# Kernel optimization log

Measured on AMD Instinct MI355X. Metric: run time of the kernel, lower is better.

The kernel has to match this reference:

```python
import jax, jax.numpy as jnp
import numpy as np

UPPER = 0.4
LOWER = 0.1
BG_RATIO = 1.0
NCLS = 20
BACKGROUND = NCLS
SIGMA = 10.0          # SmoothL1Loss(10)
MAX_POS = 2048        # fixed capacity for positive RoIs (jit-friendly)
NEGATIVE = -2
NEITHER = -1


def bbox_overlaps(b1, b2):
    """Pairwise IoU, py-faster-rcnn +1 pixel convention. b1 [L,4], b2 [M,4] -> [L,M]."""
    a1 = (b1[:, 2] - b1[:, 0] + 1.0) * (b1[:, 3] - b1[:, 1] + 1.0)  # [L]
    a2 = (b2[:, 2] - b2[:, 0] + 1.0) * (b2[:, 3] - b2[:, 1] + 1.0)  # [M]
    iw = jnp.clip(jnp.minimum(b1[:, None, 2], b2[None, :, 2]) -
                  jnp.maximum(b1[:, None, 0], b2[None, :, 0]) + 1.0, 0.0)
    ih = jnp.clip(jnp.minimum(b1[:, None, 3], b2[None, :, 3]) -
                  jnp.maximum(b1[:, None, 1], b2[None, :, 1]) + 1.0, 0.0)
    inter = iw * ih
    return inter / (a1[:, None] + a2[None, :] - inter)


def smooth_l1(d):
    s2 = SIGMA * SIGMA
    ad = jnp.abs(d)
    return jnp.where(ad < 1.0 / s2, 0.5 * s2 * d * d, ad - 0.5 / s2)


def match(pred, gt):
    """Faithful port of match(): same assignment order (upper -> gt-argmax -> lower)."""
    L = pred.shape[0]
    M = gt.shape[0]
    ov = bbox_overlaps(pred, gt)                       # [L, M]
    best_p = ov.max(axis=1)
    idx_p = ov.argmax(axis=1).astype(jnp.int32)
    ret = jnp.full((L,), NEITHER, dtype=jnp.int32)
    ret = jnp.where(best_p >= UPPER, idx_p, ret)
    idx_g = ov.argmax(axis=0)                          # [M] best roi per gt
    ret = ret.at[idx_g].set(jnp.arange(M, dtype=jnp.int32))
    ret = jnp.where(best_p < LOWER, NEGATIVE, ret)     # applied last, as in torch
    return ret


def reference(rois, cls_scores, bbox_deltas, gt_boxes, gt_cls):
    L, C = cls_scores.shape
    boxes = rois[:, 1:]                                # drop batch index column
    score_idx = jnp.argmax(cls_scores, axis=1)         # [L] predicted class per roi
    deltas = bbox_deltas.reshape(L, C, 4)
    deltas = jnp.take_along_axis(deltas, score_idx[:, None, None], axis=1)[:, 0, :]
    pred = boxes + deltas                              # [L, 4]
    gt = gt_boxes[0]                                   # [M, 4]

    matches = match(pred, gt)                          # [L] int32
    pos = matches >= 0
    neg = matches == NEGATIVE
    num_pos = pos.sum()

    # --- negative sampling: randperm(neg)[:bg_num], done via random ranks ---
    bg_num = jnp.round(num_pos.astype(jnp.float32) * BG_RATIO).astype(jnp.int32)
    u = jax.random.uniform(jax.random.key(42), (L,))
    rank = jnp.zeros((L,), jnp.int32).at[jnp.argsort(jnp.where(neg, u, 2.0))].set(
        jnp.arange(L, dtype=jnp.int32))
    sel_neg = neg & (rank < bg_num)

    # --- classification loss (mean CE over pos + sampled neg) ---
    labels = jnp.where(pos, gt_cls[jnp.clip(matches, 0)], BACKGROUND)
    w = (pos | sel_neg).astype(cls_scores.dtype)
    logp = jax.nn.log_softmax(cls_scores, axis=1)
    ce = -jnp.take_along_axis(logp, labels[:, None], axis=1)[:, 0]
    cls_loss = (ce * w).sum() / w.sum()

    # --- bbox loss over positives (fixed-capacity gather) ---
    order = jnp.argsort(jnp.where(pos, jnp.arange(L), L + jnp.arange(L)))
    pos_idx = order[:MAX_POS]
    valid = pos[pos_idx].astype(pred.dtype)            # [K]
    pred_pos = pred[pos_idx]                           # [K, 4]
    gt_pos = gt[jnp.clip(matches[pos_idx], 0)]         # [K, 4]
    # original broadcasts pred [P,4] against gt.reshape(P,1,4) -> [P,P,4]
    diff = pred_pos[None, :, :] - gt_pos[:, None, :]   # [K, K, 4]
    pair_w = valid[:, None] * valid[None, :]
    bbox_loss = (smooth_l1(diff) * pair_w[:, :, None]).sum() / 1.0  # norm = ones(1)
    return cls_loss, bbox_loss


def setup_inputs() -> dict:
    key = jax.random.key(0)
    ks = jax.random.split(key, 6)
    L, C, M = 65536, 21, 512
    SCALE = 20000.0
    wh = jax.random.uniform(ks[0], (L, 2), minval=100.0, maxval=300.0)
    xy = jax.random.uniform(ks[1], (L, 2), minval=0.0, maxval=SCALE - 300.0)
    boxes = jnp.concatenate([xy, xy + wh], axis=1)                 # [L,4]
    rois = jnp.concatenate([jnp.zeros((L, 1)), boxes], axis=1)     # [L,5]
    jitter = jax.random.uniform(ks[2], (M, 4), minval=-10.0, maxval=10.0)
    gt_boxes = (boxes[:M] + jitter)[None]                          # [1,M,4], IoU>=0.4 w/ first M rois
    gt_cls = jax.random.randint(ks[3], (M,), 0, NCLS, dtype=jnp.int32)
    cls_scores = jax.random.normal(ks[4], (L, C))
    bbox_deltas = jax.random.normal(ks[5], (L, 4 * C)) * 2.0
    return dict(rois=rois, cls_scores=cls_scores, bbox_deltas=bbox_deltas,
                gt_boxes=gt_boxes, gt_cls=gt_cls)
```

## Files before the change

### kernel.cpp

```cpp
#include <hip/hip_runtime.h>
#include <stdint.h>

typedef unsigned int u32;
typedef unsigned long long u64;

#define F_UPPER 0.4f
#define F_LOWER 0.1f
#define MAX_POS 2048
#define L_SZ 65536
#define M_SZ 512
#define C_SZ 21
#define NBINS 8192
#define BIN_CAP 32
#define OVF_CAP 1024
#define COL_TAG 0xC000000000000000ull

#define CELL_SHIFT 11
#define GRID_W 10

struct State {
  int num_pos;
  int num_neg;
  u32 done;
  u32 _pad;
  double bbox_sum;
};

__device__ __forceinline__ float area_fn(const float4 a) {
#pragma clang fp contract(off)
  return (a.z - a.x + 1.0f) * (a.w - a.y + 1.0f);
}

__device__ __forceinline__ float inter_fn(const float4 a, const float4 b) {
#pragma clang fp contract(off)
  float iw = fminf(a.z, b.z) - fmaxf(a.x, b.x) + 1.0f;
  iw = fmaxf(iw, 0.0f);
  float ih = fminf(a.w, b.w) - fmaxf(a.y, b.y) + 1.0f;
  ih = fmaxf(ih, 0.0f);
  return iw * ih;
}

__device__ __forceinline__ float iou_from_inter(float inter, float a1, float a2) {
#pragma clang fp contract(off)
  return inter * __builtin_amdgcn_rcpf(a1 + a2 - inter);
}

__device__ __forceinline__ float sl1(float d) {
#pragma clang fp contract(off)
  float ad = fabsf(d);
  return (ad < 0.01f) ? (50.0f * d * d) : (ad - 0.005f);
}

__device__ __forceinline__ int cellc(float f) {
  int c = ((int)f) >> CELL_SHIFT;
  return (c < 0) ? 0 : ((c > GRID_W - 1) ? GRID_W - 1 : c);
}

__device__ __forceinline__ u32 rotl(u32 x, int d) { return (x << d) | (x >> (32 - d)); }

__device__ u32 threefry_bits(u32 i, u32 H) {
  u32 x0, x1; bool hi;
  if (i < H) { x0 = i;     x1 = i + H; hi = false; }
  else       { x0 = i - H; x1 = i;     hi = true;  }
  const u32 ks0 = 0u, ks1 = 42u;
  const u32 ks2 = ks0 ^ ks1 ^ 0x1BD11BDAu;
  x0 += ks0; x1 += ks1;
#define RND(r) { x0 += x1; x1 = rotl(x1, r); x1 ^= x0; }
  RND(13) RND(15) RND(26) RND(6)   x0 += ks1; x1 += ks2 + 1u;
  RND(17) RND(29) RND(16) RND(24)  x0 += ks2; x1 += ks0 + 2u;
  RND(13) RND(15) RND(26) RND(6)   x0 += ks0; x1 += ks1 + 3u;
  RND(17) RND(29) RND(16) RND(24)  x0 += ks1; x1 += ks2 + 4u;
  RND(13) RND(15) RND(26) RND(6)   x0 += ks2; x1 += ks0 + 5u;
#undef RND
  return hi ? x1 : x0;
}

__global__ void __launch_bounds__(256) kA(const float* __restrict__ rois,
    const float* __restrict__ scores, const float* __restrict__ deltas,
    const float4* __restrict__ gtb,
    float4* __restrict__ pred, float* __restrict__ lse,
    u64* __restrict__ rowkey, u64* __restrict__ gkey, u32* __restrict__ hist0) {
  __shared__ __align__(16) float ssc[256 * C_SZ];
  __shared__ __align__(16) float sro[256 * 5];
  __shared__ float4 sgt[M_SZ];
  __shared__ u32    sgi[M_SZ];
  __shared__ u32    scnt[128];
  __shared__ u32    soff[130];
  __shared__ u64    scol[M_SZ];
  __shared__ u32    scarry;
  const int tid = threadIdx.x;
  const int b = blockIdx.x;
  const int i = (b << 8) + tid;
  const int lane = tid & 63;
  if (tid < 32) hist0[(b << 5) + tid] = 0u;
  {
    const float4* s4 = (const float4*)(scores + (size_t)(b << 8) * C_SZ);
    float4* d4 = (float4*)ssc;
    for (int k = tid; k < (256 * C_SZ) / 4; k += 256) d4[k] = s4[k];
    const float4* r4 = (const float4*)(rois + (size_t)(b << 8) * 5);
    float4* q4 = (float4*)sro;
    for (int k = tid; k < (256 * 5) / 4; k += 256) q4[k] = r4[k];
  }
  float4 g0 = gtb[tid];
  float4 g1 = gtb[tid + 256];
  if (tid < 128) scnt[tid] = 0u;
  scol[tid] = 0ull; scol[tid + 256] = 0ull;
  __syncthreads();
  const int c0 = cellc(g0.y) * GRID_W + cellc(g0.x);
  const int c1 = cellc(g1.y) * GRID_W + cellc(g1.x);
  atomicAdd(&scnt[c0], 1u);
  atomicAdd(&scnt[c1], 1u);
  __syncthreads();
  if (tid < 128) {
    u32 x = scnt[tid];
    for (int off = 1; off < 64; off <<= 1) {
      u32 t = __shfl_up(x, off, 64);
      if (lane >= off) x += t;
    }
    if (tid == 63) scarry = x;
    soff[tid + 1] = x;
    if (tid == 0) soff[0] = 0u;
  }
  __syncthreads();
  if (tid >= 64 && tid < 128) soff[tid + 1] += scarry;
  __syncthreads();
  if (tid < 128) scnt[tid] = soff[tid];
  __syncthreads();
  {
    u32 p0 = atomicAdd(&scnt[c0], 1u);
    sgt[p0] = g0; sgi[p0] = (u32)tid;
    u32 p1 = atomicAdd(&scnt[c1], 1u);
    sgt[p1] = g1; sgi[p1] = (u32)(tid + 256);
  }
  __syncthreads();
  const float* sr = ssc + tid * C_SZ;
  float mx = sr[0]; int mi = 0;
  for (int j = 1; j < C_SZ; ++j) { float v = sr[j]; if (v > mx) { mx = v; mi = j; } }
  float ssum = 0.0f;
  for (int j = 0; j < C_SZ; ++j) ssum += expf(sr[j] - mx);
  lse[i] = mx + logf(ssum);
  float4 d = *(const float4*)(deltas + (size_t)i * (4 * C_SZ) + 4 * mi);
  const float* r = sro + tid * 5;
  float4 p;
  p.x = r[1] + d.x; p.y = r[2] + d.y; p.z = r[3] + d.z; p.w = r[4] + d.w;
  pred[i] = p;
  const float pa = area_fn(p);
  float rbest = 0.0f; int rbj = 0;
  const int cx0 = cellc(p.x - 322.0f), cx1 = cellc(p.z + 1.0f);
  const int cy0 = cellc(p.y - 322.0f), cy1 = cellc(p.w + 1.0f);
  for (int cy = cy0; cy <= cy1; ++cy) {
    for (int cx = cx0; cx <= cx1; ++cx) {
      const int c = cy * GRID_W + cx;
      const int k1 = (int)soff[c + 1];
      for (int k = (int)soff[c]; k < k1; ++k) {
        float4 g = sgt[k];
        float inter = inter_fn(p, g);
        if (inter > 0.0f) {
          float v = iou_from_inter(inter, pa, area_fn(g));
          int j = (int)sgi[k];
          if (v > rbest) { rbest = v; rbj = j; }
          u64 ck = ((u64)__float_as_uint(v) << 32) | (u32)(0xFFFFFFFFu - (u32)i);
          atomicMax(&scol[j], ck);
        }
      }
    }
  }
  rowkey[i] = (rbest > 0.0f)
      ? (((u64)__float_as_uint(rbest) << 32) | (u32)(0xFFFFFFFFu - (u32)rbj))
      : 0ull;
  __syncthreads();
  for (int j = tid; j < M_SZ; j += 256) {
    u64 c = scol[j];
    if ((c >> 32) != 0ull) atomicMax(&gkey[j], c | COL_TAG);
  }
}

__global__ void __launch_bounds__(256) kB1(const u64* __restrict__ rowkey,
    const u64* __restrict__ gkey, const int* __restrict__ gtc,
    const float* __restrict__ scores, const float* __restrict__ lse,
    const float4* __restrict__ pred, const float4* __restrict__ gtb,
    u32* __restrict__ neg_u, u32* __restrict__ hist0, u64* __restrict__ bins,
    u32* __restrict__ blockcnt, double* __restrict__ posce,
    float4* __restrict__ ppg, float4* __restrict__ gpg, State* st) {
  __shared__ int sscat[256];
  __shared__ int swsum[4], sncnt[4];
  __shared__ double sdacc[4];
  const int tid = threadIdx.x, b = blockIdx.x;
  const int lane = tid & 63, wid = tid >> 6;
  if (b == 0 && tid == 0) { st->done = 0u; st->bbox_sum = 0.0; }
  sscat[tid] = -1;
  __syncthreads();
  for (int g = tid; g < M_SZ; g += 256) {
    u64 key = gkey[g];
    int pidx = (int)(0xFFFFFFFFu - (u32)key);
    if ((pidx >> 8) == b) atomicMax(&sscat[pidx & 255], g);
  }
  __syncthreads();
  const int i = (b << 8) + tid;
  u64 rk = rowkey[i];
  float best = __uint_as_float((u32)(rk >> 32));
  int idxp = (int)(0xFFFFFFFFu - (u32)rk);
  int m;
  if (best < F_LOWER) m = -2;
  else {
    int s = sscat[tid];
    m = (s >= 0) ? s : ((best >= F_UPPER) ? idxp : -1);
  }
  u32 ub = threefry_bits((u32)i, L_SZ >> 1) >> 9;
  neg_u[i] = (m == -2) ? ub : 0xFFFFFFFFu;
  float ce = 0.0f;
  if (m >= 0) {
    ce = lse[i] - scores[(size_t)i * C_SZ + gtc[m]];
  } else if (m == -2) {
    u32 bin = ub >> 10;
    u32 pos = atomicAdd(&hist0[bin], 1u);
    if (pos < BIN_CAP) bins[(size_t)bin * BIN_CAP + pos] = ((u64)ub << 16) | (u32)i;
  }
  const int flag = (m >= 0) ? 1 : 0;
  int incl = flag;
#pragma unroll
  for (int off = 1; off < 64; off <<= 1) {
    int x = __shfl_up(incl, off, 64);
    if (lane >= off) incl += x;
  }
  u64 baln = __ballot(m == -2);
  double acc = (double)ce;
  for (int off = 32; off > 0; off >>= 1) acc += __shfl_down(acc, off, 64);
  if (lane == 63) swsum[wid] = incl;
  if (lane == 0) { sncnt[wid] = __popcll(baln); sdacc[wid] = acc; }
  __syncthreads();
  int wbase = 0;
  for (int w = 0; w < wid; ++w) wbase += swsum[w];
  if (flag) {
    int lrank = wbase + incl - flag;
    ppg[(b << 8) + lrank] = pred[i];
    gpg[(b << 8) + lrank] = gtb[m];
  }
  if (tid == 0) {
    u32 cp = (u32)(swsum[0] + swsum[1] + swsum[2] + swsum[3]);
    u32 cn = (u32)(sncnt[0] + sncnt[1] + sncnt[2] + sncnt[3]);
    blockcnt[b] = cp | (cn << 16);
    posce[b] = sdacc[0] + sdacc[1] + sdacc[2] + sdacc[3];
  }
}

__device__ __forceinline__ int rank_src(const int* sscan, int r) {
  int lo = 0, hi = 255;
  while (lo < hi) { int mid = (lo + hi) >> 1; if (sscan[mid] > r) hi = mid; else lo = mid + 1; }
  return lo;
}

__global__ void __launch_bounds__(256) kBC2(const float4* __restrict__ ppg,
    const float4* __restrict__ gpg, const u32* __restrict__ blockcnt,
    const u32* __restrict__ hist0, const u64* __restrict__ bins,
    const u32* __restrict__ neg_u, const float* __restrict__ scores,
    const float* __restrict__ lse, const double* __restrict__ posce,
    double* __restrict__ negce, State* st, float* __restrict__ out) {
  __shared__ int sscan[256];
  __shared__ int scp[256];
  __shared__ int sncnt[4];
  __shared__ double sdacc[4];
  __shared__ int s_d, s_kk, s_cnt;
  __shared__ u32 s_ovf;
  __shared__ u64 sth;
  __shared__ u64 scand[OVF_CAP];
  __shared__ float4 sj[128];
  __shared__ int s_last;
  const int tid = threadIdx.x, b = blockIdx.x;
  const int lane = tid & 63, wid = tid >> 6;
  u32 v = blockcnt[tid];
  int cp = (int)(v & 0xFFFFu), cn = (int)(v >> 16);
  scp[tid] = cp;
  sscan[tid] = cp;
  {
    int c = cn;
    for (int off = 32; off > 0; off >>= 1) c += __shfl_down(c, off, 64);
    if (lane == 0) sncnt[wid] = c;
  }
  __syncthreads();
  for (int off = 1; off < 256; off <<= 1) {
    int x = (tid >= off) ? sscan[tid - off] : 0;
    __syncthreads();
    sscan[tid] += x;
    __syncthreads();
  }
  const int np = sscan[255];
  const int nn = sncnt[0] + sncnt[1] + sncnt[2] + sncnt[3];
  int n = np; if (n > MAX_POS) n = MAX_POS;
  float4 grow; bool irow = false;
  const int jb = (b & 15) << 7;
  if (b < 128) {
    if (tid < 128) {
      int rr = jb + tid;
      if (rr < n) {
        int s = rank_src(sscan, rr);
        int local = rr - (sscan[s] - scp[s]);
        sj[tid] = ppg[(s << 8) + local];
      } else {
        sj[tid] = make_float4(0.f, 0.f, 0.f, 0.f);
      }
    }
    const int ii = ((b >> 4) << 8) + tid;
    if (ii < n) {
      int s = rank_src(sscan, ii);
      int local = ii - (sscan[s] - scp[s]);
      grow = gpg[(s << 8) + local];
      irow = true;
    }
  }
  __syncthreads();
  u64 thresh = ~0ull;
  if (np < nn) {
    const uint4* h4 = (const uint4*)hist0;
    u32 loc[32]; int tsum = 0;
#pragma unroll
    for (int r = 0; r < 8; ++r) {
      uint4 hv = h4[tid * 8 + r];
      loc[r*4] = hv.x; loc[r*4+1] = hv.y; loc[r*4+2] = hv.z; loc[r*4+3] = hv.w;
      tsum += (int)(hv.x + hv.y + hv.z + hv.w);
    }
    sscan[tid] = tsum;
    __syncthreads();
    for (int off = 1; off < 256; off <<= 1) {
      int x = (tid >= off) ? sscan[tid - off] : 0;
      __syncthreads();
      sscan[tid] += x;
      __syncthreads();
    }
    int incl2 = sscan[tid], excl2 = incl2 - tsum;
    if (np >= excl2 && np < incl2) {
      int kk = np - excl2; int d = 0, c = 0;
#pragma unroll
      for (int r = 0; r < 32; ++r) {
        if (kk < (int)loc[r]) { d = tid * 32 + r; c = (int)loc[r]; break; }
        kk -= (int)loc[r];
      }
      s_d = d; s_kk = kk; s_cnt = c;
    }
    if (tid == 0) s_ovf = 0;
    __syncthreads();
    const int d = s_d, kk = s_kk, cnt = s_cnt;
    if (cnt <= BIN_CAP) {
      if (tid < cnt) scand[tid] = bins[(size_t)d * BIN_CAP + tid];
      __syncthreads();
      if (tid < cnt) {
        u64 key = scand[tid];
        int rank = 0;
        for (int u = 0; u < cnt; ++u) rank += (scand[u] < key) ? 1 : 0;
        if (rank == kk) sth = key;
      }
    } else {
      for (int t = tid; t < L_SZ; t += 256) {
        u32 u = neg_u[t];
        if (u != 0xFFFFFFFFu && (int)(u >> 10) == d) {
          u32 pos = atomicAdd(&s_ovf, 1u);
          if (pos < OVF_CAP) scand[pos] = ((u64)u << 16) | (u32)t;
        }
      }
      __syncthreads();
      int c2 = (int)s_ovf; if (c2 > OVF_CAP) c2 = OVF_CAP;
      for (int t = tid; t < c2; t += 256) {
        u64 key = scand[t];
        int rank = 0;
        for (int u = 0; u < c2; ++u) rank += (scand[u] < key) ? 1 : 0;
        if (rank == kk) sth = key;
      }
    }
    __syncthreads();
    thresh = sth;
  }
  {
    const int i = (b << 8) + tid;
    u32 u = neg_u[i];
    double acc = 0.0;
    if (u != 0xFFFFFFFFu) {
      u64 key = ((u64)u << 16) | (u32)i;
      if (key < thresh)
        acc = (double)(lse[i] - scores[(size_t)i * C_SZ + (C_SZ - 1)]);
    }
    for (int off = 32; off > 0; off >>= 1) acc += __shfl_down(acc, off, 64);
    if (lane == 0) sdacc[wid] = acc;
    __syncthreads();
    if (tid == 0) negce[b] = sdacc[0] + sdacc[1] + sdacc[2] + sdacc[3];
  }
  __syncthreads();
  if (b < 128) {
    double pacc = 0.0;
    if (irow) {
      int jend = n - jb; if (jend > 128) jend = 128;
      for (int j = 0; j < jend; ++j) {
        float4 p4 = sj[j];
        pacc += (double)sl1(p4.x - grow.x);
        pacc += (double)sl1(p4.y - grow.y);
        pacc += (double)sl1(p4.z - grow.z);
        pacc += (double)sl1(p4.w - grow.w);
      }
    }
    for (int off = 32; off > 0; off >>= 1) pacc += __shfl_down(pacc, off, 64);
    if (lane == 0) sdacc[wid] = pacc;
    __syncthreads();
    if (tid == 0)
      atomicAdd(&st->bbox_sum, sdacc[0] + sdacc[1] + sdacc[2] + sdacc[3]);
  }
  if (tid == 0) {
    __threadfence();
    u32 dn = atomicAdd(&st->done, 1u);
    s_last = (dn == 255u) ? 1 : 0;
  }
  __syncthreads();
  if (!s_last) return;
  __threadfence();
  double a = posce[tid] + negce[tid];
  for (int off = 32; off > 0; off >>= 1) a += __shfl_down(a, off, 64);
  if (lane == 0) sdacc[wid] = a;
  __syncthreads();
  if (tid == 0) {
    double ce = sdacc[0] + sdacc[1] + sdacc[2] + sdacc[3];
    double bbs = __hip_atomic_load(&st->bbox_sum, __ATOMIC_ACQUIRE, __HIP_MEMORY_SCOPE_AGENT);
    int nsel = (np < nn) ? np : nn;
    double wsum = (double)(np + nsel);
    out[0] = (float)(ce / wsum);
    out[1] = (float)bbs;
  }
}


extern "C" void kernel_launch(void* const* d_in, const int* in_sizes, int n_in,
                              void* d_out, int out_size, void* d_ws, size_t ws_size,
                              hipStream_t stream) {
  const float* rois   = (const float*)d_in[0];
  const float* scores = (const float*)d_in[1];
  const float* deltas = (const float*)d_in[2];
  const float4* gtb   = (const float4*)d_in[3];
  const int*   gtc    = (const int*)d_in[4];
  float* out = (float*)d_out;

  char* w = (char*)d_ws;
  State* st    = (State*)w;   w += 256;
  u64* gkey    = (u64*)w;     w += (size_t)M_SZ * 8;
  u32* hist0   = (u32*)w;     w += (size_t)NBINS * 4;
  u64* bins    = (u64*)w;     w += (size_t)NBINS * BIN_CAP * 8;
  float4* pred = (float4*)w;  w += (size_t)L_SZ * 16;
  float* lse   = (float*)w;   w += (size_t)L_SZ * 4;
  u64* rowkey  = (u64*)w;     w += (size_t)L_SZ * 8;
  u32* neg_u   = (u32*)w;     w += (size_t)L_SZ * 4;
  float4* ppg  = (float4*)w;  w += (size_t)256 * 256 * 16;
  float4* gpg  = (float4*)w;  w += (size_t)256 * 256 * 16;
  u32* blockcnt= (u32*)w;     w += 256 * 4;
  double* posce= (double*)w;  w += 256 * 8;
  double* negce= (double*)w;  w += 256 * 8;

  kA<<<L_SZ / 256, 256, 0, stream>>>(rois, scores, deltas, gtb, pred, lse, rowkey, gkey, hist0);
  kB1<<<L_SZ / 256, 256, 0, stream>>>(rowkey, gkey, gtc, scores, lse, pred, gtb,
                                      neg_u, hist0, bins, blockcnt, posce, ppg, gpg, st);
  kBC2<<<L_SZ / 256, 256, 0, stream>>>(ppg, gpg, blockcnt, hist0, bins, neg_u,
                                       scores, lse, posce, negce, st, out);
}
```

Measured before the change: 121.1 us.

## Fuse match classification into kA and collapse kB1/kBC2 via candidate list

```diff
diff --git a/kernel.cpp b/kernel.cpp
--- a/kernel.cpp
+++ b/kernel.cpp
@@ -13,16 +13,15 @@
 #define NBINS 8192
 #define BIN_CAP 32
 #define OVF_CAP 1024
+#define CAND_CAP 3072
 #define COL_TAG 0xC000000000000000ull
 
 #define CELL_SHIFT 11
 #define GRID_W 10
 
 struct State {
-  int num_pos;
-  int num_neg;
   u32 done;
-  u32 _pad;
+  u32 cand_cnt;
   double bbox_sum;
 };
 
@@ -79,7 +78,9 @@
     const float* __restrict__ scores, const float* __restrict__ deltas,
     const float4* __restrict__ gtb,
     float4* __restrict__ pred, float* __restrict__ lse,
-    u64* __restrict__ rowkey, u64* __restrict__ gkey, u32* __restrict__ hist0) {
+    u64* __restrict__ rowkey, u64* __restrict__ gkey, u32* __restrict__ hist0,
+    u64* __restrict__ bins, u32* __restrict__ neg_u, u64* __restrict__ cand,
+    State* st) {
   __shared__ __align__(16) float ssc[256 * C_SZ];
   __shared__ __align__(16) float sro[256 * 5];
   __shared__ float4 sgt[M_SZ];
@@ -92,7 +93,6 @@
   const int b = blockIdx.x;
   const int i = (b << 8) + tid;
   const int lane = tid & 63;
-  if (tid < 32) hist0[(b << 5) + tid] = 0u;
   {
     const float4* s4 = (const float4*)(scores + (size_t)(b << 8) * C_SZ);
     float4* d4 = (float4*)ssc;
@@ -168,6 +168,18 @@
   rowkey[i] = (rbest > 0.0f)
       ? (((u64)__float_as_uint(rbest) << 32) | (u32)(0xFFFFFFFFu - (u32)rbj))
       : 0ull;
+  if (rbest < F_LOWER) {
+    u32 ub = threefry_bits((u32)i, L_SZ >> 1) >> 9;
+    neg_u[i] = ub;
+    u32 bin = ub >> 10;
+    u32 pos = atomicAdd(&hist0[bin], 1u);
+    if (pos < BIN_CAP) bins[(size_t)bin * BIN_CAP + pos] = ((u64)ub << 16) | (u32)i;
+  } else {
+    neg_u[i] = 0xFFFFFFFFu;
+    u32 slot = atomicAdd(&st->cand_cnt, 1u);
+    if (slot < CAND_CAP)
+      cand[slot] = ((u64)__float_as_uint(rbest) << 32) | ((u64)(u32)i << 16) | (u32)rbj;
+  }
   __syncthreads();
   for (int j = tid; j < M_SZ; j += 256) {
     u64 c = scol[j];
@@ -175,91 +187,29 @@
   }
 }
 
-__global__ void __launch_bounds__(256) kB1(const u64* __restrict__ rowkey,
+__device__ __forceinline__ int hash_lookup(const u64* shash, u32 pidx) {
+  u32 h = (pidx * 2654435761u) >> 22;
+  for (;;) {
+    u64 cur = shash[h];
+    if (cur == 0ull) return -1;
+    if ((cur >> 16) == (u64)(pidx + 1u)) return (int)(cur & 0xFFFFull);
+    h = (h + 1u) & 1023u;
+  }
+}
+
+__global__ void __launch_bounds__(256) kB(const u64* __restrict__ cand,
     const u64* __restrict__ gkey, const int* __restrict__ gtc,
     const float* __restrict__ scores, const float* __restrict__ lse,
     const float4* __restrict__ pred, const float4* __restrict__ gtb,
-    u32* __restrict__ neg_u, u32* __restrict__ hist0, u64* __restrict__ bins,
-    u32* __restrict__ blockcnt, double* __restrict__ posce,
-    float4* __restrict__ ppg, float4* __restrict__ gpg, State* st) {
-  __shared__ int sscat[256];
-  __shared__ int swsum[4], sncnt[4];
-  __shared__ double sdacc[4];
-  const int tid = threadIdx.x, b = blockIdx.x;
-  const int lane = tid & 63, wid = tid >> 6;
-  if (b == 0 && tid == 0) { st->done = 0u; st->bbox_sum = 0.0; }
-  sscat[tid] = -1;
-  __syncthreads();
-  for (int g = tid; g < M_SZ; g += 256) {
-    u64 key = gkey[g];
-    int pidx = (int)(0xFFFFFFFFu - (u32)key);
-    if ((pidx >> 8) == b) atomicMax(&sscat[pidx & 255], g);
-  }
-  __syncthreads();
-  const int i = (b << 8) + tid;
-  u64 rk = rowkey[i];
-  float best = __uint_as_float((u32)(rk >> 32));
-  int idxp = (int)(0xFFFFFFFFu - (u32)rk);
-  int m;
-  if (best < F_LOWER) m = -2;
-  else {
-    int s = sscat[tid];
-    m = (s >= 0) ? s : ((best >= F_UPPER) ? idxp : -1);
-  }
-  u32 ub = threefry_bits((u32)i, L_SZ >> 1) >> 9;
-  neg_u[i] = (m == -2) ? ub : 0xFFFFFFFFu;
-  float ce = 0.0f;
-  if (m >= 0) {
-    ce = lse[i] - scores[(size_t)i * C_SZ + gtc[m]];
-  } else if (m == -2) {
-    u32 bin = ub >> 10;
-    u32 pos = atomicAdd(&hist0[bin], 1u);
-    if (pos < BIN_CAP) bins[(size_t)bin * BIN_CAP + pos] = ((u64)ub << 16) | (u32)i;
-  }
-  const int flag = (m >= 0) ? 1 : 0;
-  int incl = flag;
-#pragma unroll
-  for (int off = 1; off < 64; off <<= 1) {
-    int x = __shfl_up(incl, off, 64);
-    if (lane >= off) incl += x;
-  }
-  u64 baln = __ballot(m == -2);
-  double acc = (double)ce;
-  for (int off = 32; off > 0; off >>= 1) acc += __shfl_down(acc, off, 64);
-  if (lane == 63) swsum[wid] = incl;
-  if (lane == 0) { sncnt[wid] = __popcll(baln); sdacc[wid] = acc; }
-  __syncthreads();
-  int wbase = 0;
-  for (int w = 0; w < wid; ++w) wbase += swsum[w];
-  if (flag) {
-    int lrank = wbase + incl - flag;
-    ppg[(b << 8) + lrank] = pred[i];
-    gpg[(b << 8) + lrank] = gtb[m];
-  }
-  if (tid == 0) {
-    u32 cp = (u32)(swsum[0] + swsum[1] + swsum[2] + swsum[3]);
-    u32 cn = (u32)(sncnt[0] + sncnt[1] + sncnt[2] + sncnt[3]);
-    blockcnt[b] = cp | (cn << 16);
-    posce[b] = sdacc[0] + sdacc[1] + sdacc[2] + sdacc[3];
-  }
-}
-
-__device__ __forceinline__ int rank_src(const int* sscan, int r) {
-  int lo = 0, hi = 255;
-  while (lo < hi) { int mid = (lo + hi) >> 1; if (sscan[mid] > r) hi = mid; else lo = mid + 1; }
-  return lo;
-}
-
-__global__ void __launch_bounds__(256) kBC2(const float4* __restrict__ ppg,
-    const float4* __restrict__ gpg, const u32* __restrict__ blockcnt,
-    const u32* __restrict__ hist0, const u64* __restrict__ bins,
-    const u32* __restrict__ neg_u, const float* __restrict__ scores,
-    const float* __restrict__ lse, const double* __restrict__ posce,
+    const u32* __restrict__ neg_u, const u32* __restrict__ hist0,
+    const u64* __restrict__ bins, const u64* __restrict__ rowkey,
     double* __restrict__ negce, State* st, float* __restrict__ out) {
+  __shared__ u64 shash[1024];
+  __shared__ u32 cand_if[CAND_CAP];
+  __shared__ u32 posim[MAX_POS];
   __shared__ int sscan[256];
-  __shared__ int scp[256];
-  __shared__ int sncnt[4];
-  __shared__ double sdacc[4];
+  __shared__ int sint[4];
+  __shared__ double sdbl[4];
   __shared__ int s_d, s_kk, s_cnt;
   __shared__ u32 s_ovf;
   __shared__ u64 sth;
@@ -268,47 +218,128 @@
   __shared__ int s_last;
   const int tid = threadIdx.x, b = blockIdx.x;
   const int lane = tid & 63, wid = tid >> 6;
-  u32 v = blockcnt[tid];
-  int cp = (int)(v & 0xFFFFu), cn = (int)(v >> 16);
-  scp[tid] = cp;
-  sscan[tid] = cp;
-  {
-    int c = cn;
-    for (int off = 32; off > 0; off >>= 1) c += __shfl_down(c, off, 64);
-    if (lane == 0) sncnt[wid] = c;
-  }
-  __syncthreads();
-  for (int off = 1; off < 256; off <<= 1) {
-    int x = (tid >= off) ? sscan[tid - off] : 0;
-    __syncthreads();
-    sscan[tid] += x;
-    __syncthreads();
-  }
-  const int np = sscan[255];
-  const int nn = sncnt[0] + sncnt[1] + sncnt[2] + sncnt[3];
-  int n = np; if (n > MAX_POS) n = MAX_POS;
+
+  for (int k = tid; k < 1024; k += 256) shash[k] = 0ull;
+  __syncthreads();
+  for (int g = tid; g < M_SZ; g += 256) {
+    u64 key = gkey[g];
+    if ((key >> 62) != 3ull) continue;
+    u32 pidx = 0xFFFFFFFFu - (u32)key;
+    u64 comb = ((u64)(pidx + 1u) << 16) | (u32)g;
+    u32 h = (pidx * 2654435761u) >> 22;
+    for (;;) {
+      u64 cur = shash[h];
+      if (cur == 0ull) {
+        u64 prev = atomicCAS(&shash[h], 0ull, comb);
+        if (prev == 0ull) break;
+        cur = prev;
+      }
+      if ((cur >> 16) == (u64)(pidx + 1u)) { atomicMax(&shash[h], comb); break; }
+      h = (h + 1u) & 1023u;
+    }
+  }
+  __syncthreads();
+
+  const int C = (int)st->cand_cnt;
+  int np, nn;
+  double posce_loc;
+  if (C <= CAND_CAP) {
+    int cp_loc = 0; double pce = 0.0;
+    for (int c = tid; c < C; c += 256) {
+      u64 e = cand[c];
+      float kb = __uint_as_float((u32)(e >> 32));
+      u32 ci = (u32)(e >> 16) & 0xFFFFu;
+      u32 ixp = (u32)e & 0xFFFFu;
+      int g = hash_lookup(shash, ci);
+      int m = (g >= 0) ? g : ((kb >= F_UPPER) ? (int)ixp : -1);
+      cand_if[c] = (ci << 16) | (m >= 0 ? (((u32)m << 1) | 1u) : 0u);
+      if (m >= 0) {
+        cp_loc++;
+        pce += (double)(lse[ci] - scores[(size_t)ci * C_SZ + gtc[m]]);
+      }
+    }
+    __syncthreads();
+    for (int c = tid; c < C; c += 256) {
+      u32 e = cand_if[c];
+      if (e & 1u) {
+        u32 ci = e >> 16;
+        int r = 0;
+        for (int c2 = 0; c2 < C; ++c2) {
+          u32 e2 = cand_if[c2];
+          r += (int)((e2 & 1u) & (u32)((e2 >> 16) < ci));
+        }
+        if (r < MAX_POS) posim[r] = (ci << 16) | ((e >> 1) & 0x3FFu);
+      }
+    }
+    for (int off = 32; off > 0; off >>= 1) {
+      cp_loc += __shfl_down(cp_loc, off, 64);
+      pce += __shfl_down(pce, off, 64);
+    }
+    if (lane == 0) { sint[wid] = cp_loc; sdbl[wid] = pce; }
+    __syncthreads();
+    np = sint[0] + sint[1] + sint[2] + sint[3];
+    posce_loc = sdbl[0] + sdbl[1] + sdbl[2] + sdbl[3];
+    nn = L_SZ - C;
+  } else {
+    int cp_loc = 0, nn_loc = 0; double pce = 0.0;
+    const int base = tid << 8;
+    for (int k = 0; k < 256; ++k) {
+      int i = base + k;
+      u64 rk = rowkey[i];
+      float best = __uint_as_float((u32)(rk >> 32));
+      if (best < F_LOWER) { nn_loc++; continue; }
+      int ixp = (int)(0xFFFFFFFFu - (u32)rk);
+      int g = hash_lookup(shash, (u32)i);
+      int m = (g >= 0) ? g : ((best >= F_UPPER) ? ixp : -1);
+      if (m >= 0) {
+        cp_loc++;
+        pce += (double)(lse[i] - scores[(size_t)i * C_SZ + gtc[m]]);
+      }
+    }
+    sscan[tid] = cp_loc;
+    __syncthreads();
+    for (int off = 1; off < 256; off <<= 1) {
+      int x = (tid >= off) ? sscan[tid - off] : 0;
+      __syncthreads();
+      sscan[tid] += x;
+      __syncthreads();
+    }
+    np = sscan[255];
+    int r = sscan[tid] - cp_loc;
+    for (int k = 0; k < 256; ++k) {
+      int i = base + k;
+      u64 rk = rowkey[i];
+      float best = __uint_as_float((u32)(rk >> 32));
+      if (best < F_LOWER) continue;
+      int ixp = (int)(0xFFFFFFFFu - (u32)rk);
+      int g = hash_lookup(shash, (u32)i);
+      int m = (g >= 0) ? g : ((best >= F_UPPER) ? ixp : -1);
+      if (m >= 0) { if (r < MAX_POS) posim[r] = ((u32)i << 16) | (u32)m; r++; }
+    }
+    for (int off = 32; off > 0; off >>= 1) {
+      nn_loc += __shfl_down(nn_loc, off, 64);
+      pce += __shfl_down(pce, off, 64);
+    }
+    if (lane == 0) { sint[wid] = nn_loc; sdbl[wid] = pce; }
+    __syncthreads();
+    nn = sint[0] + sint[1] + sint[2] + sint[3];
+    posce_loc = sdbl[0] + sdbl[1] + sdbl[2] + sdbl[3];
+  }
+  __syncthreads();
+
+  int n = (np > MAX_POS) ? MAX_POS : np;
   float4 grow; bool irow = false;
   const int jb = (b & 15) << 7;
   if (b < 128) {
     if (tid < 128) {
       int rr = jb + tid;
-      if (rr < n) {
-        int s = rank_src(sscan, rr);
-        int local = rr - (sscan[s] - scp[s]);
-        sj[tid] = ppg[(s << 8) + local];
-      } else {
-        sj[tid] = make_float4(0.f, 0.f, 0.f, 0.f);
-      }
+      sj[tid] = (rr < n) ? pred[posim[rr] >> 16] : make_float4(0.f, 0.f, 0.f, 0.f);
     }
     const int ii = ((b >> 4) << 8) + tid;
-    if (ii < n) {
-      int s = rank_src(sscan, ii);
-      int local = ii - (sscan[s] - scp[s]);
-      grow = gpg[(s << 8) + local];
-      irow = true;
-    }
-  }
-  __syncthreads();
+    if (ii < n) { grow = gtb[posim[ii] & 0xFFFFu]; irow = true; }
+  }
+  __syncthreads();
+
   u64 thresh = ~0ull;
   if (np < nn) {
     const uint4* h4 = (const uint4*)hist0;
@@ -369,6 +400,7 @@
     __syncthreads();
     thresh = sth;
   }
+
   {
     const int i = (b << 8) + tid;
     u32 u = neg_u[i];
@@ -379,9 +411,9 @@
         acc = (double)(lse[i] - scores[(size_t)i * C_SZ + (C_SZ - 1)]);
     }
     for (int off = 32; off > 0; off >>= 1) acc += __shfl_down(acc, off, 64);
-    if (lane == 0) sdacc[wid] = acc;
-    __syncthreads();
-    if (tid == 0) negce[b] = sdacc[0] + sdacc[1] + sdacc[2] + sdacc[3];
+    if (lane == 0) sdbl[wid] = acc;
+    __syncthreads();
+    if (tid == 0) negce[b] = sdbl[0] + sdbl[1] + sdbl[2] + sdbl[3];
   }
   __syncthreads();
   if (b < 128) {
@@ -397,10 +429,10 @@
       }
     }
     for (int off = 32; off > 0; off >>= 1) pacc += __shfl_down(pacc, off, 64);
-    if (lane == 0) sdacc[wid] = pacc;
+    if (lane == 0) sdbl[wid] = pacc;
     __syncthreads();
     if (tid == 0)
-      atomicAdd(&st->bbox_sum, sdacc[0] + sdacc[1] + sdacc[2] + sdacc[3]);
+      atomicAdd(&st->bbox_sum, sdbl[0] + sdbl[1] + sdbl[2] + sdbl[3]);
   }
   if (tid == 0) {
     __threadfence();
@@ -410,16 +442,16 @@
   __syncthreads();
   if (!s_last) return;
   __threadfence();
-  double a = posce[tid] + negce[tid];
+  double a = negce[tid];
   for (int off = 32; off > 0; off >>= 1) a += __shfl_down(a, off, 64);
-  if (lane == 0) sdacc[wid] = a;
+  if (lane == 0) sdbl[wid] = a;
   __syncthreads();
   if (tid == 0) {
-    double ce = sdacc[0] + sdacc[1] + sdacc[2] + sdacc[3];
+    double negsum = sdbl[0] + sdbl[1] + sdbl[2] + sdbl[3];
     double bbs = __hip_atomic_load(&st->bbox_sum, __ATOMIC_ACQUIRE, __HIP_MEMORY_SCOPE_AGENT);
     int nsel = (np < nn) ? np : nn;
     double wsum = (double)(np + nsel);
-    out[0] = (float)(ce / wsum);
+    out[0] = (float)((posce_loc + negsum) / wsum);
     out[1] = (float)bbs;
   }
 }
@@ -437,22 +469,19 @@
 
   char* w = (char*)d_ws;
   State* st    = (State*)w;   w += 256;
+  u32* hist0   = (u32*)w;     w += (size_t)NBINS * 4;
   u64* gkey    = (u64*)w;     w += (size_t)M_SZ * 8;
-  u32* hist0   = (u32*)w;     w += (size_t)NBINS * 4;
   u64* bins    = (u64*)w;     w += (size_t)NBINS * BIN_CAP * 8;
   float4* pred = (float4*)w;  w += (size_t)L_SZ * 16;
   float* lse   = (float*)w;   w += (size_t)L_SZ * 4;
   u64* rowkey  = (u64*)w;     w += (size_t)L_SZ * 8;
   u32* neg_u   = (u32*)w;     w += (size_t)L_SZ * 4;
-  float4* ppg  = (float4*)w;  w += (size_t)256 * 256 * 16;
-  float4* gpg  = (float4*)w;  w += (size_t)256 * 256 * 16;
-  u32* blockcnt= (u32*)w;     w += 256 * 4;
-  double* posce= (double*)w;  w += 256 * 8;
+  u64* cand    = (u64*)w;     w += (size_t)CAND_CAP * 8;
   double* negce= (double*)w;  w += 256 * 8;
 
-  kA<<<L_SZ / 256, 256, 0, stream>>>(rois, scores, deltas, gtb, pred, lse, rowkey, gkey, hist0);
-  kB1<<<L_SZ / 256, 256, 0, stream>>>(rowkey, gkey, gtc, scores, lse, pred, gtb,
-                                      neg_u, hist0, bins, blockcnt, posce, ppg, gpg, st);
-  kBC2<<<L_SZ / 256, 256, 0, stream>>>(ppg, gpg, blockcnt, hist0, bins, neg_u,
-                                       scores, lse, posce, negce, st, out);
-}
+  hipMemsetAsync((void*)st, 0, 256 + (size_t)NBINS * 4, stream);
+  kA<<<L_SZ / 256, 256, 0, stream>>>(rois, scores, deltas, gtb, pred, lse, rowkey,
+                                     gkey, hist0, bins, neg_u, cand, st);
+  kB<<<L_SZ / 256, 256, 0, stream>>>(cand, gkey, gtc, scores, lse, pred, gtb,
+                                     neg_u, hist0, bins, rowkey, negce, st, out);
+}
```

After: 436.7 us. 3.6x slower.
